# Kernel optimization log

Hardware: AMD Instinct MI355X
Metric: run time of the kernel (lower is better)

Reference implementation:

```python
import jax, jax.numpy as jnp
import numpy as np

F = 32          # fmap_size = (256 // 16) * 2
WIN = F // 8 - 1  # window = 3
HID = 160
HID4 = 640
N = 4096
Q = 16


def setup_inputs() -> dict:
    key = jax.random.key(0)
    ks = jax.random.split(key, 24)

    def lin(k, i, o):
        return jax.random.normal(k, (i, o), jnp.float32) * (1.0 / np.sqrt(i))

    return {
        "feature_pos": jax.random.normal(ks[0], (N, Q, HID), jnp.float32),
        "query_embedding": jax.random.normal(ks[1], (N, Q, HID), jnp.float32),
        "attn_matrix": jax.random.normal(ks[2], (N, Q, F * F), jnp.float32),
        "ws1": lin(ks[3], HID, HID4), "bs1": jnp.zeros((HID4,), jnp.float32),
        "ws2": lin(ks[4], HID4, HID4), "bs2": jnp.zeros((HID4,), jnp.float32),
        "ws3": lin(ks[5], HID4, HID4), "bs3": jnp.zeros((HID4,), jnp.float32),
        "ws4": lin(ks[6], HID4, 1), "bs4": jnp.zeros((1,), jnp.float32),
        "wp1": lin(ks[7], HID, HID4), "bp1": jnp.zeros((HID4,), jnp.float32),
        "wp2": lin(ks[8], HID4, HID4), "bp2": jnp.zeros((HID4,), jnp.float32),
        "wp3": lin(ks[9], HID4, HID4), "bp3": jnp.zeros((HID4,), jnp.float32),
        "wp4": lin(ks[10], HID4, 4), "bp4": jnp.zeros((4,), jnp.float32),
    }


def _mlp(x, w1, b1, w2, b2, w3, b3, w4, b4):
    h = jax.nn.relu(x @ w1 + b1)
    h = jax.nn.relu(h @ w2 + b2)
    h = jax.nn.relu(h @ w3 + b3)
    return h @ w4 + b4


def _gauss_blur3(x):
    # torchvision GaussianBlur(3, sigma=1.0): separable 3-tap, reflect padding
    e = np.exp(-0.5)
    k = jnp.asarray([e, 1.0, e], jnp.float32) / np.float32(1.0 + 2.0 * e)
    xp = jnp.pad(x, ((0, 0), (1, 1), (0, 0)), mode="reflect")
    x = k[0] * xp[:, :-2] + k[1] * xp[:, 1:-1] + k[2] * xp[:, 2:]
    xp = jnp.pad(x, ((0, 0), (0, 0), (1, 1)), mode="reflect")
    return k[0] * xp[:, :, :-2] + k[1] * xp[:, :, 1:-1] + k[2] * xp[:, :, 2:]


def _process_attnmap(am):
    # am: [N, F, F]
    n = am.shape[0]
    ab = _gauss_blur3(am)
    ab = (ab - ab.mean(axis=(1, 2), keepdims=True)) / jnp.std(ab, axis=(1, 2), keepdims=True, ddof=1)
    idx = jnp.argmax(ab.reshape(n, -1), axis=1)
    px = (idx % F).astype(jnp.int32)
    py = (idx // F).astype(jnp.int32)
    # vectorized windowed mean of clamped sigmoid (masked instead of per-sample slicing)
    s = jnp.clip(jax.nn.sigmoid(am), 1e-4, 1.0 - 1e-4)
    pos = jnp.arange(F)
    colmask = ((pos[None, :] >= jnp.maximum(0, px - WIN)[:, None]) &
               (pos[None, :] < jnp.minimum(F, px + WIN)[:, None])).astype(s.dtype)  # [N,F]
    rowmask = ((pos[None, :] >= jnp.maximum(0, py - WIN)[:, None]) &
               (pos[None, :] < jnp.minimum(F, py + WIN)[:, None])).astype(s.dtype)
    colsum = s.sum(axis=1)  # [N,F] sum over rows -> per-column totals
    rowsum = s.sum(axis=2)  # [N,F] sum over cols -> per-row totals
    tempx = (colsum * colmask).sum(axis=1) / (F * colmask.sum(axis=1))
    tempy = (rowsum * rowmask).sum(axis=1) / (F * rowmask.sum(axis=1))
    prepos = jnp.stack([px, py], axis=1).astype(jnp.float32)          # [N,2]
    presize = jnp.stack([tempx, tempy], axis=1) * np.float32(F)        # [N,2]
    return prepos, presize


def reference(feature_pos, query_embedding, attn_matrix,
              ws1, bs1, ws2, bs2, ws3, bs3, ws4, bs4,
              wp1, bp1, wp2, bp2, wp3, bp3, wp4, bp4):
    n = query_embedding.shape[0]
    qe = query_embedding.mean(axis=1)   # [N, HID]
    fp = feature_pos.mean(axis=1)       # [N, HID]
    am = attn_matrix.mean(axis=1).reshape(n, F, F)
    score = _mlp(qe, ws1, bs1, ws2, bs2, ws3, bs3, ws4, bs4).reshape(n)
    bbox_info = _mlp(fp, wp1, bp1, wp2, bp2, wp3, bp3, wp4, bp4)  # [N,4]
    sizeoffset = jnp.clip(bbox_info[:, :2], -2.0, 2.0)
    posoffset = jnp.clip(bbox_info[:, 2:], -2.0, 2.0)
    prepos, presize = _process_attnmap(am)
    xy = (prepos + posoffset) / np.float32(F)
    wh = (presize + sizeoffset) / np.float32(F)
    xy = xy - 0.5 * wh  # predict_center
    bbox = jnp.concatenate([xy, wh], axis=1)
    return bbox, score
```

## Files before the change

kernel.cpp:

```cpp
#include <hip/hip_runtime.h>
#include <hip/hip_bf16.h>
#include <stdint.h>

#define HID 160
#define HID4 640
#define FDIM 32
#define NPIX 1024

#define GK0 0.27406862f
#define GK1 0.45186276f

typedef __attribute__((ext_vector_type(8))) short short8;
typedef __attribute__((ext_vector_type(4))) float f32x4;

__device__ __forceinline__ ushort f2b(float f) {
  union { float f; uint32_t u; } v; v.f = f;
  uint32_t u = v.u;
  u += 0x7fffu + ((u >> 16) & 1u);
  return (ushort)(u >> 16);
}
__device__ __forceinline__ float b2f(ushort s) {
  union { uint32_t u; float f; } v; v.u = ((uint32_t)s) << 16;
  return v.f;
}

__device__ __forceinline__ void gload16(const ushort* g, ushort* l) {
  __builtin_amdgcn_global_load_lds(
      (const __attribute__((address_space(1))) void*)g,
      (__attribute__((address_space(3))) void*)l, 16, 0, 0);
}

struct AttnSM {
  float am[FDIM][FDIM + 1];
  float tmp[FDIM][FDIM + 1];
  float bl[FDIM][FDIM + 1];
  float rowsum[FDIM], colsum[FDIM];
  float redv[4];
  int redi[4];
};

union GemmSM {
  struct {
    ushort la[128 * 160];
    ushort lb[128 * 160];
  } g;
  AttnSM a;
};

union PrepSM {
  float t[32][33];
  AttnSM a;
};

__device__ void attn_block(AttnSM& sm, const float* __restrict__ attn,
                           float* __restrict__ pp, int n) {
  const int tid = threadIdx.x;
  const float* base = attn + (size_t)n * (16 * NPIX);
  float4 a = make_float4(0.f, 0.f, 0.f, 0.f);
#pragma unroll
  for (int q = 0; q < 16; ++q) {
    float4 v = *(const float4*)(base + q * NPIX + tid * 4);
    a.x += v.x; a.y += v.y; a.z += v.z; a.w += v.w;
  }
  {
    const int f0 = tid * 4;
    const int r = f0 >> 5, c = f0 & 31;
    sm.am[r][c + 0] = a.x * 0.0625f;
    sm.am[r][c + 1] = a.y * 0.0625f;
    sm.am[r][c + 2] = a.z * 0.0625f;
    sm.am[r][c + 3] = a.w * 0.0625f;
  }
  __syncthreads();
  for (int f = tid; f < NPIX; f += 256) {
    int r = f >> 5, c = f & 31;
    int rm = (r == 0) ? 1 : r - 1;
    int rp = (r == 31) ? 30 : r + 1;
    sm.tmp[r][c] = GK0 * sm.am[rm][c] + GK1 * sm.am[r][c] + GK0 * sm.am[rp][c];
  }
  __syncthreads();
  for (int f = tid; f < NPIX; f += 256) {
    int r = f >> 5, c = f & 31;
    int cm = (c == 0) ? 1 : c - 1;
    int cp = (c == 31) ? 30 : c + 1;
    sm.bl[r][c] = GK0 * sm.tmp[r][cm] + GK1 * sm.tmp[r][c] + GK0 * sm.tmp[r][cp];
  }
  __syncthreads();
  float bv = -1e30f; int bi = 0;
  for (int f = tid; f < NPIX; f += 256) {
    float v = sm.bl[f >> 5][f & 31];
    if (v > bv || (v == bv && f < bi)) { bv = v; bi = f; }
  }
  for (int off = 32; off > 0; off >>= 1) {
    float ov = __shfl_down(bv, off);
    int oi = __shfl_down(bi, off);
    if (ov > bv || (ov == bv && oi < bi)) { bv = ov; bi = oi; }
  }
  if ((tid & 63) == 0) { sm.redv[tid >> 6] = bv; sm.redi[tid >> 6] = bi; }
  for (int f = tid; f < NPIX; f += 256) {
    int r = f >> 5, c = f & 31;
    float s = 1.f / (1.f + expf(-sm.am[r][c]));
    sm.tmp[r][c] = fminf(fmaxf(s, 1e-4f), 0.9999f);
  }
  __syncthreads();
  if (tid < 32) {
    float s = 0.f;
    for (int c = 0; c < 32; ++c) s += sm.tmp[tid][c];
    sm.rowsum[tid] = s;
  } else if (tid < 64) {
    int c = tid - 32;
    float s = 0.f;
    for (int r = 0; r < 32; ++r) s += sm.tmp[r][c];
    sm.colsum[c] = s;
  }
  __syncthreads();
  if (tid == 0) {
    float bestv = sm.redv[0]; int besti = sm.redi[0];
    for (int w = 1; w < 4; ++w)
      if (sm.redv[w] > bestv || (sm.redv[w] == bestv && sm.redi[w] < besti)) {
        bestv = sm.redv[w]; besti = sm.redi[w];
      }
    int px = besti & 31, py = besti >> 5;
    int c0 = max(0, px - 3), c1 = min(32, px + 3);
    float sx = 0.f;
    for (int c = c0; c < c1; ++c) sx += sm.colsum[c];
    float psx = (sx / (32.f * (float)(c1 - c0))) * 32.f;
    int r0 = max(0, py - 3), r1 = min(32, py + 3);
    float sy = 0.f;
    for (int r = r0; r < r1; ++r) sy += sm.rowsum[r];
    float psy = (sy / (32.f * (float)(r1 - r0))) * 32.f;
    pp[n * 4 + 0] = (float)px;
    pp[n * 4 + 1] = (float)py;
    pp[n * 4 + 2] = psx;
    pp[n * 4 + 3] = psy;
  }
}

template <int K>
__global__ __launch_bounds__(256, 2) void gemm_attn(
    const ushort* __restrict__ A0, const ushort* __restrict__ A1,
    const ushort* __restrict__ W0, const ushort* __restrict__ W1,
    const float* __restrict__ B0, const float* __restrict__ B1,
    ushort* __restrict__ O0, ushort* __restrict__ O1,
    const float* __restrict__ attn, float* __restrict__ pp,
    int attn_base, int n_gemm) {
  __shared__ GemmSM sm;
  const int tid = threadIdx.x;

  if ((int)blockIdx.x >= n_gemm) {
    attn_block(sm.a, attn, pp, attn_base + (int)blockIdx.x - n_gemm);
    return;
  }

  const int bid = blockIdx.x;
  const int half = n_gemm >> 1;
  const int chain = bid >= half;
  const int r = chain ? bid - half : bid;
  const int bn = (r % 5) * 128;
  const int bm = (r / 5) * 128;
  const ushort* A = chain ? A1 : A0;
  const ushort* W = chain ? W1 : W0;
  const float* bias = chain ? B1 : B0;
  ushort* O = chain ? O1 : O0;

  const int lane = tid & 63;
  const int wid = tid >> 6;
  const int wr = (wid >> 1) * 64;
  const int wc = (wid & 1) * 64;
  const int l15 = lane & 15;
  const int kq = (lane >> 4) * 8;

  ushort* la = sm.g.la;
  ushort* lb = sm.g.lb;

  uint offA[10], offB[10];
#pragma unroll
  for (int i = 0; i < 10; ++i) {
    const uint e = (uint)(wid * 10 + i) * 512 + lane * 8;
    const uint row = e / 160;
    const uint col = e - row * 160;
    offA[i] = (uint)(bm + row) * K + col;
    offB[i] = (uint)(bn + row) * K + col;
  }

  constexpr int NT = K / 160;
  f32x4 acc[4][4] = {};
  for (int t = 0; t < NT; ++t) {
    const int k0 = t * 160;
#pragma unroll
    for (int i = 0; i < 10; ++i) {
      const int ldso = (wid * 10 + i) * 512;
      gload16(A + offA[i] + k0, la + ldso);
      gload16(W + offB[i] + k0, lb + ldso);
    }
    __syncthreads();
#pragma unroll
    for (int ks = 0; ks < 5; ++ks) {
      short8 af[4], bf[4];
#pragma unroll
      for (int i = 0; i < 4; ++i) {
        af[i] = *(const short8*)(la + (wr + i * 16 + l15) * 160 + ks * 32 + kq);
        bf[i] = *(const short8*)(lb + (wc + i * 16 + l15) * 160 + ks * 32 + kq);
      }
#pragma unroll
      for (int mi = 0; mi < 4; ++mi)
#pragma unroll
        for (int nj = 0; nj < 4; ++nj)
          acc[mi][nj] = __builtin_amdgcn_mfma_f32_16x16x32_bf16(af[mi], bf[nj], acc[mi][nj], 0, 0, 0);
    }
    if (t + 1 < NT) __syncthreads();
  }

#pragma unroll
  for (int nj = 0; nj < 4; ++nj) {
    const int col = bn + wc + nj * 16 + l15;
    const float bcol = bias[col];
#pragma unroll
    for (int mi = 0; mi < 4; ++mi) {
      const int rbase = bm + wr + mi * 16 + (lane >> 4) * 4;
#pragma unroll
      for (int b = 0; b < 4; ++b) {
        float v = acc[mi][nj][b] + bcol;
        O[(size_t)(rbase + b) * HID4 + col] = f2b(fmaxf(v, 0.f));
      }
    }
  }
}

__global__ __launch_bounds__(256, 4) void prep_kernel(
    const float* __restrict__ qemb, const float* __restrict__ fpos,
    ushort* __restrict__ qe_b, ushort* __restrict__ fp_b,
    const float* __restrict__ ws1, ushort* __restrict__ wts1,
    const float* __restrict__ wp1, ushort* __restrict__ wtp1,
    const float* __restrict__ ws2, ushort* __restrict__ wts2,
    const float* __restrict__ wp2, ushort* __restrict__ wtp2,
    const float* __restrict__ ws3, ushort* __restrict__ wts3,
    const float* __restrict__ wp3, ushort* __restrict__ wtp3,
    const float* __restrict__ attn, float* __restrict__ pp,
    int n_mean_blocks, int n_trans_blocks, int total) {
  __shared__ PrepSM sm;
  const int tid = threadIdx.x;
  const int bid = blockIdx.x;

  if (bid < n_mean_blocks) {
    int idx = bid * 256 + tid;
    const int pairs = total >> 1;
    const float* src; ushort* dst; int i;
    if (idx < pairs) { src = qemb; dst = qe_b; i = idx; }
    else             { src = fpos; dst = fp_b; i = idx - pairs; }
    int nn = i / (HID / 2);
    int h = (i - nn * (HID / 2)) * 2;
    const float* p = src + (size_t)nn * (16 * HID) + h;
    float sx = 0.f, sy = 0.f;
#pragma unroll
    for (int q = 0; q < 16; ++q) {
      float2 v = *(const float2*)(p + q * HID);
      sx += v.x; sy += v.y;
    }
    ushort2 o;
    o.x = f2b(sx * 0.0625f);
    o.y = f2b(sy * 0.0625f);
    *(ushort2*)(dst + (size_t)nn * HID + h) = o;
    return;
  }

  if (bid < n_mean_blocks + n_trans_blocks) {
    int r = bid - n_mean_blocks;
    const float* in; ushort* out; int K;
    if (r < 100)       { in = ws1; out = wts1; K = HID; }
    else if (r < 200)  { in = wp1; out = wtp1; K = HID; r -= 100; }
    else if (r < 600)  { in = ws2; out = wts2; K = HID4; r -= 200; }
    else if (r < 1000) { in = wp2; out = wtp2; K = HID4; r -= 600; }
    else if (r < 1400) { in = ws3; out = wts3; K = HID4; r -= 1000; }
    else               { in = wp3; out = wtp3; K = HID4; r -= 1400; }
    const int bx = (r % 20) * 32;
    const int by = (r / 20) * 32;
    const int lx = tid & 31;
    const int ly = tid >> 5;
#pragma unroll
    for (int i = 0; i < 4; ++i)
      sm.t[ly + i * 8][lx] = in[(size_t)(by + ly + i * 8) * HID4 + bx + lx];
    __syncthreads();
#pragma unroll
    for (int i = 0; i < 4; ++i)
      out[(size_t)(bx + ly + i * 8) * K + by + lx] = f2b(sm.t[lx][ly + i * 8]);
    return;
  }

  attn_block(sm.a, attn, pp, bid - n_mean_blocks - n_trans_blocks);
}

__global__ __launch_bounds__(256) void final_kernel(
    const ushort* __restrict__ hs, const ushort* __restrict__ hp,
    const float* __restrict__ ws4, const float* __restrict__ bs4,
    const float* __restrict__ wp4, const float* __restrict__ bp4,
    const float* __restrict__ pp, float* __restrict__ out, int N) {
  const int wid = threadIdx.x >> 6;
  const int lane = threadIdx.x & 63;
  const int n = blockIdx.x * 4 + wid;
  if (n >= N) return;
  const ushort* hsr = hs + (size_t)n * HID4;
  const ushort* hpr = hp + (size_t)n * HID4;
  float sc = 0.f, b0 = 0.f, b1 = 0.f, b2 = 0.f, b3 = 0.f;
  for (int j = lane; j < HID4; j += 64) {
    float h1 = b2f(hsr[j]);
    sc += h1 * ws4[j];
    float h2 = b2f(hpr[j]);
    b0 += h2 * wp4[j * 4 + 0];
    b1 += h2 * wp4[j * 4 + 1];
    b2 += h2 * wp4[j * 4 + 2];
    b3 += h2 * wp4[j * 4 + 3];
  }
  for (int off = 32; off > 0; off >>= 1) {
    sc += __shfl_down(sc, off);
    b0 += __shfl_down(b0, off);
    b1 += __shfl_down(b1, off);
    b2 += __shfl_down(b2, off);
    b3 += __shfl_down(b3, off);
  }
  if (lane == 0) {
    sc += bs4[0];
    b0 += bp4[0]; b1 += bp4[1]; b2 += bp4[2]; b3 += bp4[3];
    float so0 = fminf(fmaxf(b0, -2.f), 2.f);
    float so1 = fminf(fmaxf(b1, -2.f), 2.f);
    float po0 = fminf(fmaxf(b2, -2.f), 2.f);
    float po1 = fminf(fmaxf(b3, -2.f), 2.f);
    float px = pp[n * 4 + 0], py = pp[n * 4 + 1];
    float psx = pp[n * 4 + 2], psy = pp[n * 4 + 3];
    float wh0 = (psx + so0) * (1.f / 32.f);
    float wh1 = (psy + so1) * (1.f / 32.f);
    float xy0 = (px + po0) * (1.f / 32.f) - 0.5f * wh0;
    float xy1 = (py + po1) * (1.f / 32.f) - 0.5f * wh1;
    out[n * 4 + 0] = xy0;
    out[n * 4 + 1] = xy1;
    out[n * 4 + 2] = wh0;
    out[n * 4 + 3] = wh1;
    out[(size_t)4 * N + n] = sc;
  }
}

extern "C" void kernel_launch(void* const* d_in, const int* in_sizes, int n_in,
                              void* d_out, int out_size, void* d_ws, size_t ws_size,
                              hipStream_t stream) {
  const float* fpos = (const float*)d_in[0];
  const float* qemb = (const float*)d_in[1];
  const float* attn = (const float*)d_in[2];
  const float* ws1 = (const float*)d_in[3];
  const float* bs1 = (const float*)d_in[4];
  const float* ws2 = (const float*)d_in[5];
  const float* bs2 = (const float*)d_in[6];
  const float* ws3 = (const float*)d_in[7];
  const float* bs3 = (const float*)d_in[8];
  const float* ws4 = (const float*)d_in[9];
  const float* bs4 = (const float*)d_in[10];
  const float* wp1 = (const float*)d_in[11];
  const float* bp1 = (const float*)d_in[12];
  const float* wp2 = (const float*)d_in[13];
  const float* bp2 = (const float*)d_in[14];
  const float* wp3 = (const float*)d_in[15];
  const float* bp3 = (const float*)d_in[16];
  const float* wp4 = (const float*)d_in[17];
  const float* bp4 = (const float*)d_in[18];
  float* out = (float*)d_out;

  const int N = in_sizes[0] / (16 * HID);

  char* ws = (char*)d_ws;
  const size_t SZ_QE = (size_t)N * HID * 2;
  const size_t SZ_W1 = (size_t)HID4 * HID * 2;
  const size_t SZ_W2 = (size_t)HID4 * HID4 * 2;
  const size_t SZ_H  = (size_t)N * HID4 * 2;
  size_t off = 0;
  ushort* qe_b = (ushort*)(ws + off); off += SZ_QE;
  ushort* fp_b = (ushort*)(ws + off); off += SZ_QE;
  ushort* wts1 = (ushort*)(ws + off); off += SZ_W1;
  ushort* wtp1 = (ushort*)(ws + off); off += SZ_W1;
  ushort* wts2 = (ushort*)(ws + off); off += SZ_W2;
  ushort* wtp2 = (ushort*)(ws + off); off += SZ_W2;
  ushort* wts3 = (ushort*)(ws + off); off += SZ_W2;
  ushort* wtp3 = (ushort*)(ws + off); off += SZ_W2;
  ushort* hsA  = (ushort*)(ws + off); off += SZ_H;
  ushort* hsB  = (ushort*)(ws + off); off += SZ_H;
  ushort* hpA  = (ushort*)(ws + off); off += SZ_H;
  ushort* hpB  = (ushort*)(ws + off); off += SZ_H;
  float*  pp   = (float*)(ws + off);  off += (size_t)N * 4 * 4;

  const int a1 = 350;
  const int a2 = 600;
  const int a3 = 600;
  const int a0 = N - a1 - a2 - a3;

  const int total = N * HID;
  const int n_mean = (total + 255) / 256;
  const int n_trans = 1800;
  prep_kernel<<<n_mean + n_trans + a0, 256, 0, stream>>>(
      qemb, fpos, qe_b, fp_b, ws1, wts1, wp1, wtp1, ws2, wts2, wp2, wtp2,
      ws3, wts3, wp3, wtp3, attn, pp, n_mean, n_trans, total);

  const int n_gemm = 2 * (N / 128) * (HID4 / 128);

  gemm_attn<HID><<<n_gemm + a1, 256, 0, stream>>>(
      qe_b, fp_b, wts1, wtp1, bs1, bp1, hsA, hpA, attn, pp, a0, n_gemm);
  gemm_attn<HID4><<<n_gemm + a2, 256, 0, stream>>>(
      hsA, hpA, wts2, wtp2, bs2, bp2, hsB, hpB, attn, pp, a0 + a1, n_gemm);
  gemm_attn<HID4><<<n_gemm + a3, 256, 0, stream>>>(
      hsB, hpB, wts3, wtp3, bs3, bp3, hsA, hpA, attn, pp, a0 + a1 + a2, n_gemm);

  final_kernel<<<(N + 3) / 4, 256, 0, stream>>>(hsA, hpA, ws4, bs4, wp4, bp4, pp, out, N);
}
```

Baseline: 126.4 us.

## Replace LDS-staged 128x128 GEMM with direct-load 64x64 tiles, rebalance attn blocks

The GEMM kernel drops LDS staging through global_load_lds and instead has each wave load A and W fragments straight from global memory into registers. Each block now computes a 64x64 tile, with each wave owning 16 columns, and occupancy hints rise to 8 blocks per CU. The attention-map blocks are moved out of the prep kernel and spread across the three GEMM launches, and the attention load loop is split by a sched barrier. The aim is more parallelism and less LDS and sync overhead, at the cost of more redundant global and L2 traffic for A, since all four waves reload the same A rows.

```diff
diff --git a/kernel.cpp b/kernel.cpp
--- a/kernel.cpp
+++ b/kernel.cpp
@@ -22,12 +22,6 @@
 __device__ __forceinline__ float b2f(ushort s) {
   union { uint32_t u; float f; } v; v.u = ((uint32_t)s) << 16;
   return v.f;
-}
-
-__device__ __forceinline__ void gload16(const ushort* g, ushort* l) {
-  __builtin_amdgcn_global_load_lds(
-      (const __attribute__((address_space(1))) void*)g,
-      (__attribute__((address_space(3))) void*)l, 16, 0, 0);
 }
 
 struct AttnSM {
@@ -39,26 +33,19 @@
   int redi[4];
 };
 
-union GemmSM {
-  struct {
-    ushort la[128 * 160];
-    ushort lb[128 * 160];
-  } g;
-  AttnSM a;
-};
-
-union PrepSM {
-  float t[32][33];
-  AttnSM a;
-};
-
 __device__ void attn_block(AttnSM& sm, const float* __restrict__ attn,
                            float* __restrict__ pp, int n) {
   const int tid = threadIdx.x;
   const float* base = attn + (size_t)n * (16 * NPIX);
   float4 a = make_float4(0.f, 0.f, 0.f, 0.f);
 #pragma unroll
-  for (int q = 0; q < 16; ++q) {
+  for (int q = 0; q < 8; ++q) {
+    float4 v = *(const float4*)(base + q * NPIX + tid * 4);
+    a.x += v.x; a.y += v.y; a.z += v.z; a.w += v.w;
+  }
+  __builtin_amdgcn_sched_barrier(0);
+#pragma unroll
+  for (int q = 8; q < 16; ++q) {
     float4 v = *(const float4*)(base + q * NPIX + tid * 4);
     a.x += v.x; a.y += v.y; a.z += v.z; a.w += v.w;
   }
@@ -136,27 +123,27 @@
 }
 
 template <int K>
-__global__ __launch_bounds__(256, 2) void gemm_attn(
+__global__ __launch_bounds__(256, 8) void gemm_attn(
     const ushort* __restrict__ A0, const ushort* __restrict__ A1,
     const ushort* __restrict__ W0, const ushort* __restrict__ W1,
     const float* __restrict__ B0, const float* __restrict__ B1,
     ushort* __restrict__ O0, ushort* __restrict__ O1,
     const float* __restrict__ attn, float* __restrict__ pp,
     int attn_base, int n_gemm) {
-  __shared__ GemmSM sm;
+  __shared__ AttnSM sm;
   const int tid = threadIdx.x;
-
-  if ((int)blockIdx.x >= n_gemm) {
-    attn_block(sm.a, attn, pp, attn_base + (int)blockIdx.x - n_gemm);
+  const int bid = blockIdx.x;
+
+  if (bid >= n_gemm) {
+    attn_block(sm, attn, pp, attn_base + bid - n_gemm);
     return;
   }
 
-  const int bid = blockIdx.x;
   const int half = n_gemm >> 1;
   const int chain = bid >= half;
-  const int r = chain ? bid - half : bid;
-  const int bn = (r % 5) * 128;
-  const int bm = (r / 5) * 128;
+  const int rr = chain ? bid - half : bid;
+  const int bn = (rr % 10) * 64;
+  const int bm = (rr / 10) * 64;
   const ushort* A = chain ? A1 : A0;
   const ushort* W = chain ? W1 : W0;
   const float* bias = chain ? B1 : B0;
@@ -164,69 +151,41 @@
 
   const int lane = tid & 63;
   const int wid = tid >> 6;
-  const int wr = (wid >> 1) * 64;
-  const int wc = (wid & 1) * 64;
+  const int wc = wid * 16;
   const int l15 = lane & 15;
   const int kq = (lane >> 4) * 8;
 
-  ushort* la = sm.g.la;
-  ushort* lb = sm.g.lb;
-
-  uint offA[10], offB[10];
-#pragma unroll
-  for (int i = 0; i < 10; ++i) {
-    const uint e = (uint)(wid * 10 + i) * 512 + lane * 8;
-    const uint row = e / 160;
-    const uint col = e - row * 160;
-    offA[i] = (uint)(bm + row) * K + col;
-    offB[i] = (uint)(bn + row) * K + col;
-  }
-
-  constexpr int NT = K / 160;
-  f32x4 acc[4][4] = {};
-  for (int t = 0; t < NT; ++t) {
-    const int k0 = t * 160;
-#pragma unroll
-    for (int i = 0; i < 10; ++i) {
-      const int ldso = (wid * 10 + i) * 512;
-      gload16(A + offA[i] + k0, la + ldso);
-      gload16(W + offB[i] + k0, lb + ldso);
+  const ushort* Ab = A + (size_t)(bm + l15) * K + kq;
+  const ushort* Wb = W + (size_t)(bn + wc + l15) * K + kq;
+
+  f32x4 acc[4] = {};
+#pragma unroll 4
+  for (int k0 = 0; k0 < K; k0 += 32) {
+    short8 bf = *(const short8*)(Wb + k0);
+    short8 af0 = *(const short8*)(Ab + k0);
+    short8 af1 = *(const short8*)(Ab + 16 * K + k0);
+    short8 af2 = *(const short8*)(Ab + 32 * K + k0);
+    short8 af3 = *(const short8*)(Ab + 48 * K + k0);
+    acc[0] = __builtin_amdgcn_mfma_f32_16x16x32_bf16(af0, bf, acc[0], 0, 0, 0);
+    acc[1] = __builtin_amdgcn_mfma_f32_16x16x32_bf16(af1, bf, acc[1], 0, 0, 0);
+    acc[2] = __builtin_amdgcn_mfma_f32_16x16x32_bf16(af2, bf, acc[2], 0, 0, 0);
+    acc[3] = __builtin_amdgcn_mfma_f32_16x16x32_bf16(af3, bf, acc[3], 0, 0, 0);
+  }
+
+  const int col = bn + wc + l15;
+  const float bcol = bias[col];
+#pragma unroll
+  for (int mi = 0; mi < 4; ++mi) {
+    const int rbase = bm + mi * 16 + (lane >> 4) * 4;
+#pragma unroll
+    for (int b = 0; b < 4; ++b) {
+      float v = acc[mi][b] + bcol;
+      O[(size_t)(rbase + b) * HID4 + col] = f2b(fmaxf(v, 0.f));
     }
-    __syncthreads();
-#pragma unroll
-    for (int ks = 0; ks < 5; ++ks) {
-      short8 af[4], bf[4];
-#pragma unroll
-      for (int i = 0; i < 4; ++i) {
-        af[i] = *(const short8*)(la + (wr + i * 16 + l15) * 160 + ks * 32 + kq);
-        bf[i] = *(const short8*)(lb + (wc + i * 16 + l15) * 160 + ks * 32 + kq);
-      }
-#pragma unroll
-      for (int mi = 0; mi < 4; ++mi)
-#pragma unroll
-        for (int nj = 0; nj < 4; ++nj)
-          acc[mi][nj] = __builtin_amdgcn_mfma_f32_16x16x32_bf16(af[mi], bf[nj], acc[mi][nj], 0, 0, 0);
-    }
-    if (t + 1 < NT) __syncthreads();
-  }
-
-#pragma unroll
-  for (int nj = 0; nj < 4; ++nj) {
-    const int col = bn + wc + nj * 16 + l15;
-    const float bcol = bias[col];
-#pragma unroll
-    for (int mi = 0; mi < 4; ++mi) {
-      const int rbase = bm + wr + mi * 16 + (lane >> 4) * 4;
-#pragma unroll
-      for (int b = 0; b < 4; ++b) {
-        float v = acc[mi][nj][b] + bcol;
-        O[(size_t)(rbase + b) * HID4 + col] = f2b(fmaxf(v, 0.f));
-      }
-    }
-  }
-}
-
-__global__ __launch_bounds__(256, 4) void prep_kernel(
+  }
+}
+
+__global__ __launch_bounds__(256) void prep_kernel(
     const float* __restrict__ qemb, const float* __restrict__ fpos,
     ushort* __restrict__ qe_b, ushort* __restrict__ fp_b,
     const float* __restrict__ ws1, ushort* __restrict__ wts1,
@@ -235,9 +194,8 @@
     const float* __restrict__ wp2, ushort* __restrict__ wtp2,
     const float* __restrict__ ws3, ushort* __restrict__ wts3,
     const float* __restrict__ wp3, ushort* __restrict__ wtp3,
-    const float* __restrict__ attn, float* __restrict__ pp,
-    int n_mean_blocks, int n_trans_blocks, int total) {
-  __shared__ PrepSM sm;
+    int n_mean_blocks, int total) {
+  __shared__ float t[32][33];
   const int tid = threadIdx.x;
   const int bid = blockIdx.x;
 
@@ -263,30 +221,25 @@
     return;
   }
 
-  if (bid < n_mean_blocks + n_trans_blocks) {
-    int r = bid - n_mean_blocks;
-    const float* in; ushort* out; int K;
-    if (r < 100)       { in = ws1; out = wts1; K = HID; }
-    else if (r < 200)  { in = wp1; out = wtp1; K = HID; r -= 100; }
-    else if (r < 600)  { in = ws2; out = wts2; K = HID4; r -= 200; }
-    else if (r < 1000) { in = wp2; out = wtp2; K = HID4; r -= 600; }
-    else if (r < 1400) { in = ws3; out = wts3; K = HID4; r -= 1000; }
-    else               { in = wp3; out = wtp3; K = HID4; r -= 1400; }
-    const int bx = (r % 20) * 32;
-    const int by = (r / 20) * 32;
-    const int lx = tid & 31;
-    const int ly = tid >> 5;
-#pragma unroll
-    for (int i = 0; i < 4; ++i)
-      sm.t[ly + i * 8][lx] = in[(size_t)(by + ly + i * 8) * HID4 + bx + lx];
-    __syncthreads();
-#pragma unroll
-    for (int i = 0; i < 4; ++i)
-      out[(size_t)(bx + ly + i * 8) * K + by + lx] = f2b(sm.t[lx][ly + i * 8]);
-    return;
-  }
-
-  attn_block(sm.a, attn, pp, bid - n_mean_blocks - n_trans_blocks);
+  int r = bid - n_mean_blocks;
+  const float* in; ushort* out; int K;
+  if (r < 100)       { in = ws1; out = wts1; K = HID; }
+  else if (r < 200)  { in = wp1; out = wtp1; K = HID; r -= 100; }
+  else if (r < 600)  { in = ws2; out = wts2; K = HID4; r -= 200; }
+  else if (r < 1000) { in = wp2; out = wtp2; K = HID4; r -= 600; }
+  else if (r < 1400) { in = ws3; out = wts3; K = HID4; r -= 1000; }
+  else               { in = wp3; out = wtp3; K = HID4; r -= 1400; }
+  const int bx = (r % 20) * 32;
+  const int by = (r / 20) * 32;
+  const int lx = tid & 31;
+  const int ly = tid >> 5;
+#pragma unroll
+  for (int i = 0; i < 4; ++i)
+    t[ly + i * 8][lx] = in[(size_t)(by + ly + i * 8) * HID4 + bx + lx];
+  __syncthreads();
+#pragma unroll
+  for (int i = 0; i < 4; ++i)
+    out[(size_t)(bx + ly + i * 8) * K + by + lx] = f2b(t[lx][ly + i * 8]);
 }
 
 __global__ __launch_bounds__(256) void final_kernel(
@@ -384,26 +337,25 @@
   ushort* hpB  = (ushort*)(ws + off); off += SZ_H;
   float*  pp   = (float*)(ws + off);  off += (size_t)N * 4 * 4;
 
-  const int a1 = 350;
-  const int a2 = 600;
-  const int a3 = 600;
-  const int a0 = N - a1 - a2 - a3;
-
   const int total = N * HID;
   const int n_mean = (total + 255) / 256;
   const int n_trans = 1800;
-  prep_kernel<<<n_mean + n_trans + a0, 256, 0, stream>>>(
+  prep_kernel<<<n_mean + n_trans, 256, 0, stream>>>(
       qemb, fpos, qe_b, fp_b, ws1, wts1, wp1, wtp1, ws2, wts2, wp2, wtp2,
-      ws3, wts3, wp3, wtp3, attn, pp, n_mean, n_trans, total);
-
-  const int n_gemm = 2 * (N / 128) * (HID4 / 128);
+      ws3, wts3, wp3, wtp3, n_mean, total);
+
+  const int n_gemm = 2 * (N / 64) * (HID4 / 64);
+
+  const int a1 = 1500;
+  const int a2 = 1298;
+  const int a3 = N - a1 - a2;
 
   gemm_attn<HID><<<n_gemm + a1, 256, 0, stream>>>(
-      qe_b, fp_b, wts1, wtp1, bs1, bp1, hsA, hpA, attn, pp, a0, n_gemm);
+      qe_b, fp_b, wts1, wtp1, bs1, bp1, hsA, hpA, attn, pp, 0, n_gemm);
   gemm_attn<HID4><<<n_gemm + a2, 256, 0, stream>>>(
-      hsA, hpA, wts2, wtp2, bs2, bp2, hsB, hpB, attn, pp, a0 + a1, n_gemm);
+      hsA, hpA, wts2, wtp2, bs2, bp2, hsB, hpB, attn, pp, a1, n_gemm);
   gemm_attn<HID4><<<n_gemm + a3, 256, 0, stream>>>(
-      hsB, hpB, wts3, wtp3, bs3, bp3, hsA, hpA, attn, pp, a0 + a1 + a2, n_gemm);
+      hsB, hpB, wts3, wtp3, bs3, bp3, hsA, hpA, attn, pp, a1 + a2, n_gemm);
 
   final_kernel<<<(N + 3) / 4, 256, 0, stream>>>(hsA, hpA, ws4, bs4, wp4, bp4, pp, out, N);
 }
```

Result: slower. 195.6 us (+54.7%).

## Double-buffer GEMM K-tiles of 32 and move attention blocks out of prep

Applied to the files above, without the earlier changes.

The GEMM main loop now stages K in 32-wide tiles with two LDS buffers, prefetching the next tile via global_load_lds while MFMAs run on the current one, synchronized with explicit vmcnt waits and barriers. This shrinks LDS from 80KB to 32KB per block, which should raise occupancy, and drops the launch_bounds minimum-block hints. The attention-map blocks are taken out of prep_kernel and spread over the three GEMM launches in a new split. The trade-off is more barriers per K step and many small 16-byte load batches instead of large 160-wide tiles.

```diff
diff --git a/kernel.cpp b/kernel.cpp
--- a/kernel.cpp
+++ b/kernel.cpp
@@ -41,14 +41,9 @@
 
 union GemmSM {
   struct {
-    ushort la[128 * 160];
-    ushort lb[128 * 160];
+    ushort la[2][4096];
+    ushort lb[2][4096];
   } g;
-  AttnSM a;
-};
-
-union PrepSM {
-  float t[32][33];
   AttnSM a;
 };
 
@@ -136,7 +131,7 @@
 }
 
 template <int K>
-__global__ __launch_bounds__(256, 2) void gemm_attn(
+__global__ __launch_bounds__(256) void gemm_attn(
     const ushort* __restrict__ A0, const ushort* __restrict__ A1,
     const ushort* __restrict__ W0, const ushort* __restrict__ W1,
     const float* __restrict__ B0, const float* __restrict__ B1,
@@ -169,45 +164,52 @@
   const int l15 = lane & 15;
   const int kq = (lane >> 4) * 8;
 
-  ushort* la = sm.g.la;
-  ushort* lb = sm.g.lb;
-
-  uint offA[10], offB[10];
-#pragma unroll
-  for (int i = 0; i < 10; ++i) {
-    const uint e = (uint)(wid * 10 + i) * 512 + lane * 8;
-    const uint row = e / 160;
-    const uint col = e - row * 160;
-    offA[i] = (uint)(bm + row) * K + col;
-    offB[i] = (uint)(bn + row) * K + col;
-  }
-
-  constexpr int NT = K / 160;
+  const int rstage = tid >> 2;
+  const int cstage = (tid & 3) * 8;
+  const int ldsbase = wid * 512;
+
+  const size_t arow0 = (size_t)(bm + rstage) * K + cstage;
+  const size_t arow1 = (size_t)(bm + 64 + rstage) * K + cstage;
+  const size_t wrow0 = (size_t)(bn + rstage) * K + cstage;
+  const size_t wrow1 = (size_t)(bn + 64 + rstage) * K + cstage;
+
+  gload16(A + arow0, &sm.g.la[0][0] + ldsbase);
+  gload16(W + wrow0, &sm.g.lb[0][0] + ldsbase);
+  gload16(A + arow1, &sm.g.la[0][2048] + ldsbase);
+  gload16(W + wrow1, &sm.g.lb[0][2048] + ldsbase);
+
+  constexpr int NT = K / 32;
   f32x4 acc[4][4] = {};
   for (int t = 0; t < NT; ++t) {
-    const int k0 = t * 160;
-#pragma unroll
-    for (int i = 0; i < 10; ++i) {
-      const int ldso = (wid * 10 + i) * 512;
-      gload16(A + offA[i] + k0, la + ldso);
-      gload16(W + offB[i] + k0, lb + ldso);
+    const int cur = t & 1;
+    if (t + 1 < NT) {
+      const int k1 = (t + 1) * 32;
+      const int nxt = cur ^ 1;
+      gload16(A + arow0 + k1, &sm.g.la[nxt][0] + ldsbase);
+      gload16(W + wrow0 + k1, &sm.g.lb[nxt][0] + ldsbase);
+      gload16(A + arow1 + k1, &sm.g.la[nxt][2048] + ldsbase);
+      gload16(W + wrow1 + k1, &sm.g.lb[nxt][2048] + ldsbase);
+      asm volatile("s_waitcnt vmcnt(4)" ::: "memory");
+    } else {
+      asm volatile("s_waitcnt vmcnt(0)" ::: "memory");
     }
-    __syncthreads();
-#pragma unroll
-    for (int ks = 0; ks < 5; ++ks) {
-      short8 af[4], bf[4];
-#pragma unroll
-      for (int i = 0; i < 4; ++i) {
-        af[i] = *(const short8*)(la + (wr + i * 16 + l15) * 160 + ks * 32 + kq);
-        bf[i] = *(const short8*)(lb + (wc + i * 16 + l15) * 160 + ks * 32 + kq);
-      }
-#pragma unroll
-      for (int mi = 0; mi < 4; ++mi)
-#pragma unroll
-        for (int nj = 0; nj < 4; ++nj)
-          acc[mi][nj] = __builtin_amdgcn_mfma_f32_16x16x32_bf16(af[mi], bf[nj], acc[mi][nj], 0, 0, 0);
+    __builtin_amdgcn_s_barrier();
+
+    const ushort* lac = &sm.g.la[cur][0];
+    const ushort* lbc = &sm.g.lb[cur][0];
+    short8 af[4], bf[4];
+#pragma unroll
+    for (int i = 0; i < 4; ++i) {
+      af[i] = *(const short8*)(lac + (wr + i * 16 + l15) * 32 + kq);
+      bf[i] = *(const short8*)(lbc + (wc + i * 16 + l15) * 32 + kq);
     }
-    if (t + 1 < NT) __syncthreads();
+#pragma unroll
+    for (int mi = 0; mi < 4; ++mi)
+#pragma unroll
+      for (int nj = 0; nj < 4; ++nj)
+        acc[mi][nj] = __builtin_amdgcn_mfma_f32_16x16x32_bf16(af[mi], bf[nj], acc[mi][nj], 0, 0, 0);
+
+    __builtin_amdgcn_s_barrier();
   }
 
 #pragma unroll
@@ -226,7 +228,7 @@
   }
 }
 
-__global__ __launch_bounds__(256, 4) void prep_kernel(
+__global__ __launch_bounds__(256) void prep_kernel(
     const float* __restrict__ qemb, const float* __restrict__ fpos,
     ushort* __restrict__ qe_b, ushort* __restrict__ fp_b,
     const float* __restrict__ ws1, ushort* __restrict__ wts1,
@@ -235,9 +237,8 @@
     const float* __restrict__ wp2, ushort* __restrict__ wtp2,
     const float* __restrict__ ws3, ushort* __restrict__ wts3,
     const float* __restrict__ wp3, ushort* __restrict__ wtp3,
-    const float* __restrict__ attn, float* __restrict__ pp,
-    int n_mean_blocks, int n_trans_blocks, int total) {
-  __shared__ PrepSM sm;
+    int n_mean_blocks, int total) {
+  __shared__ float t[32][33];
   const int tid = threadIdx.x;
   const int bid = blockIdx.x;
 
@@ -263,30 +264,25 @@
     return;
   }
 
-  if (bid < n_mean_blocks + n_trans_blocks) {
-    int r = bid - n_mean_blocks;
-    const float* in; ushort* out; int K;
-    if (r < 100)       { in = ws1; out = wts1; K = HID; }
-    else if (r < 200)  { in = wp1; out = wtp1; K = HID; r -= 100; }
-    else if (r < 600)  { in = ws2; out = wts2; K = HID4; r -= 200; }
-    else if (r < 1000) { in = wp2; out = wtp2; K = HID4; r -= 600; }
-    else if (r < 1400) { in = ws3; out = wts3; K = HID4; r -= 1000; }
-    else               { in = wp3; out = wtp3; K = HID4; r -= 1400; }
-    const int bx = (r % 20) * 32;
-    const int by = (r / 20) * 32;
-    const int lx = tid & 31;
-    const int ly = tid >> 5;
-#pragma unroll
-    for (int i = 0; i < 4; ++i)
-      sm.t[ly + i * 8][lx] = in[(size_t)(by + ly + i * 8) * HID4 + bx + lx];
-    __syncthreads();
-#pragma unroll
-    for (int i = 0; i < 4; ++i)
-      out[(size_t)(bx + ly + i * 8) * K + by + lx] = f2b(sm.t[lx][ly + i * 8]);
-    return;
-  }
-
-  attn_block(sm.a, attn, pp, bid - n_mean_blocks - n_trans_blocks);
+  int r = bid - n_mean_blocks;
+  const float* in; ushort* out; int K;
+  if (r < 100)       { in = ws1; out = wts1; K = HID; }
+  else if (r < 200)  { in = wp1; out = wtp1; K = HID; r -= 100; }
+  else if (r < 600)  { in = ws2; out = wts2; K = HID4; r -= 200; }
+  else if (r < 1000) { in = wp2; out = wtp2; K = HID4; r -= 600; }
+  else if (r < 1400) { in = ws3; out = wts3; K = HID4; r -= 1000; }
+  else               { in = wp3; out = wtp3; K = HID4; r -= 1400; }
+  const int bx = (r % 20) * 32;
+  const int by = (r / 20) * 32;
+  const int lx = tid & 31;
+  const int ly = tid >> 5;
+#pragma unroll
+  for (int i = 0; i < 4; ++i)
+    t[ly + i * 8][lx] = in[(size_t)(by + ly + i * 8) * HID4 + bx + lx];
+  __syncthreads();
+#pragma unroll
+  for (int i = 0; i < 4; ++i)
+    out[(size_t)(bx + ly + i * 8) * K + by + lx] = f2b(t[lx][ly + i * 8]);
 }
 
 __global__ __launch_bounds__(256) void final_kernel(
@@ -384,26 +380,25 @@
   ushort* hpB  = (ushort*)(ws + off); off += SZ_H;
   float*  pp   = (float*)(ws + off);  off += (size_t)N * 4 * 4;
 
-  const int a1 = 350;
-  const int a2 = 600;
-  const int a3 = 600;
-  const int a0 = N - a1 - a2 - a3;
-
   const int total = N * HID;
   const int n_mean = (total + 255) / 256;
   const int n_trans = 1800;
-  prep_kernel<<<n_mean + n_trans + a0, 256, 0, stream>>>(
+  prep_kernel<<<n_mean + n_trans, 256, 0, stream>>>(
       qemb, fpos, qe_b, fp_b, ws1, wts1, wp1, wtp1, ws2, wts2, wp2, wtp2,
-      ws3, wts3, wp3, wtp3, attn, pp, n_mean, n_trans, total);
+      ws3, wts3, wp3, wtp3, n_mean, total);
 
   const int n_gemm = 2 * (N / 128) * (HID4 / 128);
 
+  const int a2 = (N * 29) / 100;
+  const int a3 = a2;
+  const int a1 = N - a2 - a3;
+
   gemm_attn<HID><<<n_gemm + a1, 256, 0, stream>>>(
-      qe_b, fp_b, wts1, wtp1, bs1, bp1, hsA, hpA, attn, pp, a0, n_gemm);
+      qe_b, fp_b, wts1, wtp1, bs1, bp1, hsA, hpA, attn, pp, 0, n_gemm);
   gemm_attn<HID4><<<n_gemm + a2, 256, 0, stream>>>(
-      hsA, hpA, wts2, wtp2, bs2, bp2, hsB, hpB, attn, pp, a0 + a1, n_gemm);
+      hsA, hpA, wts2, wtp2, bs2, bp2, hsB, hpB, attn, pp, a1, n_gemm);
   gemm_attn<HID4><<<n_gemm + a3, 256, 0, stream>>>(
-      hsB, hpB, wts3, wtp3, bs3, bp3, hsA, hpA, attn, pp, a0 + a1 + a2, n_gemm);
+      hsB, hpB, wts3, wtp3, bs3, bp3, hsA, hpA, attn, pp, a1 + a2, n_gemm);
 
   final_kernel<<<(N + 3) / 4, 256, 0, stream>>>(hsA, hpA, ws4, bs4, wp4, bp4, pp, out, N);
 }
```

After: 120.0 us. -5.1%, faster.

## Fuse three MLP GEMM layers into one kernel keeping activations in LDS

Applied to the files above, without the earlier changes.

Replaces the three separate tiled GEMM launches, which were interleaved with attention-map blocks, with one kernel. Each block processes 16 rows through all three layers, keeping the intermediate activations in swizzled LDS and streaming weights directly from global memory into MFMA operands. All attention-map processing moves into the prep kernel. This removes intermediate activation round-trips and two launches. The cost is that weights are re-read from global/L2 by every 16-row block with no LDS staging, and the attention work no longer overlaps with the GEMMs.

```diff
diff --git a/kernel.cpp b/kernel.cpp
--- a/kernel.cpp
+++ b/kernel.cpp
@@ -6,6 +6,7 @@
 #define HID4 640
 #define FDIM 32
 #define NPIX 1024
+#define MLPROWS 16
 
 #define GK0 0.27406862f
 #define GK1 0.45186276f
@@ -22,12 +23,6 @@
 __device__ __forceinline__ float b2f(ushort s) {
   union { uint32_t u; float f; } v; v.u = ((uint32_t)s) << 16;
   return v.f;
-}
-
-__device__ __forceinline__ void gload16(const ushort* g, ushort* l) {
-  __builtin_amdgcn_global_load_lds(
-      (const __attribute__((address_space(1))) void*)g,
-      (__attribute__((address_space(3))) void*)l, 16, 0, 0);
 }
 
 struct AttnSM {
@@ -37,14 +32,6 @@
   float rowsum[FDIM], colsum[FDIM];
   float redv[4];
   int redi[4];
-};
-
-union GemmSM {
-  struct {
-    ushort la[128 * 160];
-    ushort lb[128 * 160];
-  } g;
-  AttnSM a;
 };
 
 union PrepSM {
@@ -135,98 +122,7 @@
   }
 }
 
-template <int K>
-__global__ __launch_bounds__(256, 2) void gemm_attn(
-    const ushort* __restrict__ A0, const ushort* __restrict__ A1,
-    const ushort* __restrict__ W0, const ushort* __restrict__ W1,
-    const float* __restrict__ B0, const float* __restrict__ B1,
-    ushort* __restrict__ O0, ushort* __restrict__ O1,
-    const float* __restrict__ attn, float* __restrict__ pp,
-    int attn_base, int n_gemm) {
-  __shared__ GemmSM sm;
-  const int tid = threadIdx.x;
-
-  if ((int)blockIdx.x >= n_gemm) {
-    attn_block(sm.a, attn, pp, attn_base + (int)blockIdx.x - n_gemm);
-    return;
-  }
-
-  const int bid = blockIdx.x;
-  const int half = n_gemm >> 1;
-  const int chain = bid >= half;
-  const int r = chain ? bid - half : bid;
-  const int bn = (r % 5) * 128;
-  const int bm = (r / 5) * 128;
-  const ushort* A = chain ? A1 : A0;
-  const ushort* W = chain ? W1 : W0;
-  const float* bias = chain ? B1 : B0;
-  ushort* O = chain ? O1 : O0;
-
-  const int lane = tid & 63;
-  const int wid = tid >> 6;
-  const int wr = (wid >> 1) * 64;
-  const int wc = (wid & 1) * 64;
-  const int l15 = lane & 15;
-  const int kq = (lane >> 4) * 8;
-
-  ushort* la = sm.g.la;
-  ushort* lb = sm.g.lb;
-
-  uint offA[10], offB[10];
-#pragma unroll
-  for (int i = 0; i < 10; ++i) {
-    const uint e = (uint)(wid * 10 + i) * 512 + lane * 8;
-    const uint row = e / 160;
-    const uint col = e - row * 160;
-    offA[i] = (uint)(bm + row) * K + col;
-    offB[i] = (uint)(bn + row) * K + col;
-  }
-
-  constexpr int NT = K / 160;
-  f32x4 acc[4][4] = {};
-  for (int t = 0; t < NT; ++t) {
-    const int k0 = t * 160;
-#pragma unroll
-    for (int i = 0; i < 10; ++i) {
-      const int ldso = (wid * 10 + i) * 512;
-      gload16(A + offA[i] + k0, la + ldso);
-      gload16(W + offB[i] + k0, lb + ldso);
-    }
-    __syncthreads();
-#pragma unroll
-    for (int ks = 0; ks < 5; ++ks) {
-      short8 af[4], bf[4];
-#pragma unroll
-      for (int i = 0; i < 4; ++i) {
-        af[i] = *(const short8*)(la + (wr + i * 16 + l15) * 160 + ks * 32 + kq);
-        bf[i] = *(const short8*)(lb + (wc + i * 16 + l15) * 160 + ks * 32 + kq);
-      }
-#pragma unroll
-      for (int mi = 0; mi < 4; ++mi)
-#pragma unroll
-        for (int nj = 0; nj < 4; ++nj)
-          acc[mi][nj] = __builtin_amdgcn_mfma_f32_16x16x32_bf16(af[mi], bf[nj], acc[mi][nj], 0, 0, 0);
-    }
-    if (t + 1 < NT) __syncthreads();
-  }
-
-#pragma unroll
-  for (int nj = 0; nj < 4; ++nj) {
-    const int col = bn + wc + nj * 16 + l15;
-    const float bcol = bias[col];
-#pragma unroll
-    for (int mi = 0; mi < 4; ++mi) {
-      const int rbase = bm + wr + mi * 16 + (lane >> 4) * 4;
-#pragma unroll
-      for (int b = 0; b < 4; ++b) {
-        float v = acc[mi][nj][b] + bcol;
-        O[(size_t)(rbase + b) * HID4 + col] = f2b(fmaxf(v, 0.f));
-      }
-    }
-  }
-}
-
-__global__ __launch_bounds__(256, 4) void prep_kernel(
+__global__ __launch_bounds__(256) void prep_attn_kernel(
     const float* __restrict__ qemb, const float* __restrict__ fpos,
     ushort* __restrict__ qe_b, ushort* __restrict__ fp_b,
     const float* __restrict__ ws1, ushort* __restrict__ wts1,
@@ -287,6 +183,124 @@
   }
 
   attn_block(sm.a, attn, pp, bid - n_mean_blocks - n_trans_blocks);
+}
+
+__global__ __launch_bounds__(256) void mlp3_kernel(
+    const ushort* __restrict__ qe_b, const ushort* __restrict__ fp_b,
+    const ushort* __restrict__ wts1, const ushort* __restrict__ wtp1,
+    const float* __restrict__ bs1, const float* __restrict__ bp1,
+    const ushort* __restrict__ wts2, const ushort* __restrict__ wtp2,
+    const float* __restrict__ bs2, const float* __restrict__ bp2,
+    const ushort* __restrict__ wts3, const ushort* __restrict__ wtp3,
+    const float* __restrict__ bs3, const float* __restrict__ bp3,
+    ushort* __restrict__ hsA, ushort* __restrict__ hpA, int nblk_chain) {
+  __shared__ ushort hA[MLPROWS * HID4];
+  __shared__ ushort hB[MLPROWS * HID4];
+
+  const int bid = blockIdx.x;
+  const int chain = bid >= nblk_chain;
+  const int blk = chain ? bid - nblk_chain : bid;
+  const int n0 = blk * MLPROWS;
+  const ushort* A  = chain ? fp_b : qe_b;
+  const ushort* W1 = chain ? wtp1 : wts1;
+  const ushort* W2 = chain ? wtp2 : wts2;
+  const ushort* W3 = chain ? wtp3 : wts3;
+  const float* B1 = chain ? bp1 : bs1;
+  const float* B2 = chain ? bp2 : bs2;
+  const float* B3 = chain ? bp3 : bs3;
+  ushort* O = chain ? hpA : hsA;
+
+  const int tid = threadIdx.x;
+  const int lane = tid & 63;
+  const int wid = tid >> 6;
+  const int l15 = lane & 15;
+  const int kq = (lane >> 4) * 8;
+  const int rq = (lane >> 4) * 4;
+
+  for (int i = tid; i < (MLPROWS * HID) / 8; i += 256) {
+    int row = i / 20, seg = i % 20;
+    *(short8*)(&hB[row * 168 + seg * 8]) =
+        *(const short8*)(A + (size_t)(n0 + row) * HID + seg * 8);
+  }
+  __syncthreads();
+
+  f32x4 acc[10];
+
+#pragma unroll
+  for (int s = 0; s < 10; ++s) acc[s] = (f32x4){0.f, 0.f, 0.f, 0.f};
+  for (int k0 = 0; k0 < HID; k0 += 32) {
+    short8 af = *(const short8*)(&hB[l15 * 168 + k0 + kq]);
+#pragma unroll
+    for (int s = 0; s < 10; ++s) {
+      const int col = (wid + s * 4) * 16 + l15;
+      short8 bf = *(const short8*)(W1 + (size_t)col * HID + k0 + kq);
+      acc[s] = __builtin_amdgcn_mfma_f32_16x16x32_bf16(af, bf, acc[s], 0, 0, 0);
+    }
+  }
+  __syncthreads();
+#pragma unroll
+  for (int s = 0; s < 10; ++s) {
+    const int colb = (wid + s * 4) * 16;
+    const float bc = B1[colb + l15];
+#pragma unroll
+    for (int b = 0; b < 4; ++b) {
+      const int row = rq + b;
+      float v = fmaxf(acc[s][b] + bc, 0.f);
+      int ba = (row * 1280 + (colb + l15) * 2) ^ ((row & 7) << 4);
+      hA[ba >> 1] = f2b(v);
+    }
+  }
+  __syncthreads();
+
+#pragma unroll
+  for (int s = 0; s < 10; ++s) acc[s] = (f32x4){0.f, 0.f, 0.f, 0.f};
+  for (int k0 = 0; k0 < HID4; k0 += 32) {
+    int ba = (l15 * 1280 + (k0 + kq) * 2) ^ ((l15 & 7) << 4);
+    short8 af = *(const short8*)((const char*)hA + ba);
+#pragma unroll
+    for (int s = 0; s < 10; ++s) {
+      const int col = (wid + s * 4) * 16 + l15;
+      short8 bf = *(const short8*)(W2 + (size_t)col * HID4 + k0 + kq);
+      acc[s] = __builtin_amdgcn_mfma_f32_16x16x32_bf16(af, bf, acc[s], 0, 0, 0);
+    }
+  }
+#pragma unroll
+  for (int s = 0; s < 10; ++s) {
+    const int colb = (wid + s * 4) * 16;
+    const float bc = B2[colb + l15];
+#pragma unroll
+    for (int b = 0; b < 4; ++b) {
+      const int row = rq + b;
+      float v = fmaxf(acc[s][b] + bc, 0.f);
+      int ba = (row * 1280 + (colb + l15) * 2) ^ ((row & 7) << 4);
+      hB[ba >> 1] = f2b(v);
+    }
+  }
+  __syncthreads();
+
+#pragma unroll
+  for (int s = 0; s < 10; ++s) acc[s] = (f32x4){0.f, 0.f, 0.f, 0.f};
+  for (int k0 = 0; k0 < HID4; k0 += 32) {
+    int ba = (l15 * 1280 + (k0 + kq) * 2) ^ ((l15 & 7) << 4);
+    short8 af = *(const short8*)((const char*)hB + ba);
+#pragma unroll
+    for (int s = 0; s < 10; ++s) {
+      const int col = (wid + s * 4) * 16 + l15;
+      short8 bf = *(const short8*)(W3 + (size_t)col * HID4 + k0 + kq);
+      acc[s] = __builtin_amdgcn_mfma_f32_16x16x32_bf16(af, bf, acc[s], 0, 0, 0);
+    }
+  }
+#pragma unroll
+  for (int s = 0; s < 10; ++s) {
+    const int colb = (wid + s * 4) * 16;
+    const float bc = B3[colb + l15];
+#pragma unroll
+    for (int b = 0; b < 4; ++b) {
+      const int row = rq + b;
+      float v = fmaxf(acc[s][b] + bc, 0.f);
+      O[(size_t)(n0 + row) * HID4 + colb + l15] = f2b(v);
+    }
+  }
 }
 
 __global__ __launch_bounds__(256) void final_kernel(
@@ -379,31 +393,20 @@
   ushort* wts3 = (ushort*)(ws + off); off += SZ_W2;
   ushort* wtp3 = (ushort*)(ws + off); off += SZ_W2;
   ushort* hsA  = (ushort*)(ws + off); off += SZ_H;
-  ushort* hsB  = (ushort*)(ws + off); off += SZ_H;
   ushort* hpA  = (ushort*)(ws + off); off += SZ_H;
-  ushort* hpB  = (ushort*)(ws + off); off += SZ_H;
   float*  pp   = (float*)(ws + off);  off += (size_t)N * 4 * 4;
-
-  const int a1 = 350;
-  const int a2 = 600;
-  const int a3 = 600;
-  const int a0 = N - a1 - a2 - a3;
 
   const int total = N * HID;
   const int n_mean = (total + 255) / 256;
   const int n_trans = 1800;
-  prep_kernel<<<n_mean + n_trans + a0, 256, 0, stream>>>(
+  prep_attn_kernel<<<n_mean + n_trans + N, 256, 0, stream>>>(
       qemb, fpos, qe_b, fp_b, ws1, wts1, wp1, wtp1, ws2, wts2, wp2, wtp2,
       ws3, wts3, wp3, wtp3, attn, pp, n_mean, n_trans, total);
 
-  const int n_gemm = 2 * (N / 128) * (HID4 / 128);
-
-  gemm_attn<HID><<<n_gemm + a1, 256, 0, stream>>>(
-      qe_b, fp_b, wts1, wtp1, bs1, bp1, hsA, hpA, attn, pp, a0, n_gemm);
-  gemm_attn<HID4><<<n_gemm + a2, 256, 0, stream>>>(
-      hsA, hpA, wts2, wtp2, bs2, bp2, hsB, hpB, attn, pp, a0 + a1, n_gemm);
-  gemm_attn<HID4><<<n_gemm + a3, 256, 0, stream>>>(
-      hsB, hpB, wts3, wtp3, bs3, bp3, hsA, hpA, attn, pp, a0 + a1 + a2, n_gemm);
+  const int nblk_chain = N / MLPROWS;
+  mlp3_kernel<<<2 * nblk_chain, 256, 0, stream>>>(
+      qe_b, fp_b, wts1, wtp1, bs1, bp1, wts2, wtp2, bs2, bp2,
+      wts3, wtp3, bs3, bp3, hsA, hpA, nblk_chain);
 
   final_kernel<<<(N + 3) / 4, 256, 0, stream>>>(hsA, hpA, ws4, bs4, wp4, bp4, pp, out, N);
 }
```

New measurement: 179.0 us. 41.6% more time.
